# Performance work log

Hardware: AMD Instinct MI355X
Metric: run time of the kernel (lower is better)

The kernel has to match this reference:

```python
import jax, jax.numpy as jnp
import numpy as np

N = 50000
NUM_GRAPHS = 64
EPS = 1e-16  # PyG softmax denominator epsilon


def _gat_conv(x, src, dst, W, a_src, a_dst, b, heads, out_ch):
    n = x.shape[0]
    h = (x @ W).reshape(n, heads, out_ch)                    # [N,H,C]
    al_s = jnp.einsum('nhc,hc->nh', h, a_src)                # [N,H]
    al_d = jnp.einsum('nhc,hc->nh', h, a_dst)                # [N,H]
    e = jax.nn.leaky_relu(al_s[src] + al_d[dst], 0.2)        # [E,H]
    emax = jax.ops.segment_max(e, dst, num_segments=n)       # [N,H]
    ee = jnp.exp(e - emax[dst])
    den = jax.ops.segment_sum(ee, dst, num_segments=n)       # [N,H]
    alpha = ee / (den[dst] + EPS)                            # [E,H]
    msg = h[src] * alpha[:, :, None]                         # [E,H,C]
    out = jax.ops.segment_sum(msg, dst, num_segments=n)      # [N,H,C]
    return out.reshape(n, heads * out_ch) + b


def setup_inputs() -> dict:
    key = jax.random.key(0)
    ks = jax.random.split(key, 16)
    E = 250000
    x = jax.random.normal(ks[0], (N, 11), dtype=jnp.float32)
    edge_index = jax.random.randint(ks[1], (2, E), 0, N, dtype=jnp.int64)
    batch = jnp.sort(jax.random.randint(ks[2], (N,), 0, NUM_GRAPHS, dtype=jnp.int64))
    def glorot(k, shape):
        fan = shape[0] + shape[-1]
        return jax.random.uniform(k, shape, jnp.float32, -1.0, 1.0) * np.sqrt(6.0 / fan)
    return {
        'x': x, 'edge_index': edge_index, 'batch': batch,
        'W1': glorot(ks[3], (11, 8 * 128)),
        'a1s': glorot(ks[4], (8, 128)), 'a1d': glorot(ks[5], (8, 128)),
        'b1': jnp.zeros((8 * 128,), jnp.float32),
        'W2': glorot(ks[6], (1024, 8 * 64)),
        'a2s': glorot(ks[7], (8, 64)), 'a2d': glorot(ks[8], (8, 64)),
        'b2': jnp.zeros((8 * 64,), jnp.float32),
        'W3': glorot(ks[9], (512, 4 * 32)),
        'a3s': glorot(ks[10], (4, 32)), 'a3d': glorot(ks[11], (4, 32)),
        'b3': jnp.zeros((4 * 32,), jnp.float32),
        'Wout': glorot(ks[12], (128, 1)),
        'bout': jnp.zeros((1,), jnp.float32),
    }


def reference(x, edge_index, batch, W1, a1s, a1d, b1, W2, a2s, a2d, b2,
              W3, a3s, a3d, b3, Wout, bout):
    n = x.shape[0]
    # GATConv adds self-loops by default
    loop = jnp.arange(n, dtype=edge_index.dtype)
    src = jnp.concatenate([edge_index[0], loop])
    dst = jnp.concatenate([edge_index[1], loop])
    h = jax.nn.leaky_relu(_gat_conv(x, src, dst, W1, a1s, a1d, b1, 8, 128), 0.01)
    h = jax.nn.leaky_relu(_gat_conv(h, src, dst, W2, a2s, a2d, b2, 8, 64), 0.01)
    h = jax.nn.leaky_relu(_gat_conv(h, src, dst, W3, a3s, a3d, b3, 4, 32), 0.01)
    # global mean pool over graphs
    sums = jax.ops.segment_sum(h, batch, num_segments=NUM_GRAPHS)      # [G,128]
    cnt = jax.ops.segment_sum(jnp.ones((n,), h.dtype), batch, num_segments=NUM_GRAPHS)
    pooled = sums / jnp.maximum(cnt, 1.0)[:, None]
    return pooled @ Wout + bout                                        # [G,1]
```

## Files before the change

### kernel.cpp

```cpp
#include <hip/hip_runtime.h>

#define EPS 1e-16f

typedef __attribute__((ext_vector_type(8))) short short8;
typedef __attribute__((ext_vector_type(4))) float f32x4;

__device__ __forceinline__ float b2f(unsigned short u) {
    return __uint_as_float(((unsigned)u) << 16);
}
__device__ __forceinline__ unsigned short f2b(float f) {
    unsigned u = __float_as_uint(f);
    u += 0x7fffu + ((u >> 16) & 1u);
    return (unsigned short)(u >> 16);
}

typedef __attribute__((address_space(3))) void lds_vp;
typedef __attribute__((address_space(1))) const void glb_vp;
__device__ __forceinline__ void load_lds16(const unsigned short* g,
                                           unsigned short* l) {
    __builtin_amdgcn_global_load_lds((glb_vp*)g, (lds_vp*)l, 16, 0, 0);
}

__global__ void setup_kernel(const float* __restrict__ W1,
                             const float* __restrict__ W2,
                             const float* __restrict__ W3,
                             unsigned short* __restrict__ wt2,
                             unsigned short* __restrict__ wt3,
                             unsigned short* __restrict__ w1sk,
                             const float* __restrict__ a1s,
                             const float* __restrict__ a1d,
                             float* __restrict__ w_as,
                             float* __restrict__ w_ad, int* __restrict__ deg,
                             float* __restrict__ pool, int N, int GC, int WB,
                             int DB, int PB) {
    int b = blockIdx.x, t = threadIdx.x;
    if (b < WB) {
        int i = b * 256 + t;
        if (i < 1024 * 512) {
            int k = i / 512, n = i % 512;
            wt2[(size_t)n * 1024 + k] = f2b(W2[i]);
        } else if (i < 1024 * 512 + 512 * 128) {
            int j = i - 1024 * 512;
            int k = j / 128, n = j % 128;
            wt3[(size_t)n * 512 + k] = f2b(W3[j]);
        } else if (i < 1024 * 512 + 512 * 128 + 8 * 128 * 32) {
            int q = i - (1024 * 512 + 512 * 128);
            int h = q >> 12, rem = q & 4095;
            int c = rem >> 5, kk = rem & 31;
            int off = (h == 7) ? 16 : 0;
            float v = 0.f;
            int k = kk - off;
            if (k >= 0 && k < 11) v = W1[k * 1024 + h * 128 + c];
            w1sk[q] = f2b(v);
        }
    } else if (b < WB + DB) {
        int i = (b - WB) * 256 + t;
        if (i < N) deg[i] = 1;
    } else if (b < WB + DB + PB) {
        int i = (b - WB - DB) * 256 + t;
        if (i < GC) pool[i] = 0.f;
    } else {
        if (t < 88) {
            int h = t / 11, k = t % 11;
            float s = 0.f, d = 0.f;
            for (int c = 0; c < 128; c++) {
                float w = W1[k * 1024 + h * 128 + c];
                s += w * a1s[h * 128 + c];
                d += w * a1d[h * 128 + c];
            }
            w_as[h * 16 + k] = s;
            w_ad[h * 16 + k] = d;
        }
    }
}

__global__ void hist_al1_kernel(const int* __restrict__ ei, int E, int N,
                                int* __restrict__ deg,
                                const float* __restrict__ x,
                                const float* __restrict__ w_as,
                                const float* __restrict__ w_ad,
                                float* __restrict__ als,
                                float* __restrict__ ald, int EB) {
    int b = blockIdx.x, t = threadIdx.x;
    if (b < EB) {
        int e = b * 256 + t;
        if (e < E) {
            int d = ei[E + e];
            if ((unsigned)d < (unsigned)N) atomicAdd(&deg[d], 1);
        }
    } else {
        int i = (b - EB) * 256 + t;
        if (i < N * 8) {
            int n = i >> 3, h = i & 7;
            float s = 0.f, d = 0.f;
#pragma unroll
            for (int k = 0; k < 11; k++) {
                float xv = x[n * 11 + k];
                s += xv * w_as[h * 16 + k];
                d += xv * w_ad[h * 16 + k];
            }
            als[i] = s;
            ald[i] = d;
        }
    }
}

__global__ void scan_block_kernel(const int* __restrict__ deg,
                                  int* __restrict__ rowst,
                                  int* __restrict__ bsum, int N) {
    __shared__ int s[256];
    int t = threadIdx.x, b = blockIdx.x;
    int i = b * 256 + t;
    s[t] = (i < N) ? deg[i] : 0;
    __syncthreads();
    for (int o = 1; o < 256; o <<= 1) {
        int a = (t >= o) ? s[t - o] : 0;
        __syncthreads();
        s[t] += a;
        __syncthreads();
    }
    if (i < N) rowst[i + 1] = s[t];
    if (t == 255) bsum[b] = s[255];
}

__global__ void scan_top_kernel(const int* __restrict__ bsum,
                                int* __restrict__ boff, int NB) {
    __shared__ int psum[65];
    int t = threadIdx.x;
    int chunk = (NB + 63) / 64;
    int lo = t * chunk, hi = lo + chunk;
    if (lo > NB) lo = NB;
    if (hi > NB) hi = NB;
    int s = 0;
    for (int i = lo; i < hi; i++) s += bsum[i];
    psum[t + 1] = s;
    __syncthreads();
    if (t == 0) {
        psum[0] = 0;
        for (int i = 1; i <= 64; i++) psum[i] += psum[i - 1];
    }
    __syncthreads();
    int run = psum[t];
    for (int i = lo; i < hi; i++) {
        boff[i] = run;
        run += bsum[i];
    }
}

__global__ void scan_finish_kernel(int* __restrict__ rowst,
                                   const int* __restrict__ boff,
                                   const int* __restrict__ deg,
                                   int* __restrict__ srcs,
                                   int* __restrict__ cursor, int N) {
    int i = blockIdx.x * 256 + threadIdx.x;
    if (i == 0) rowst[0] = 0;
    if (i < N) {
        int incl = rowst[i + 1] + boff[blockIdx.x];
        rowst[i + 1] = incl;
        int st = incl - deg[i];
        srcs[st] = i;
        cursor[i] = st + 1;
    }
}

__global__ void scatter_kernel(const int* __restrict__ ei, int E, int N,
                               int* cursor, int* srcs) {
    int e = blockIdx.x * blockDim.x + threadIdx.x;
    if (e < E) {
        int d = ei[E + e];
        if ((unsigned)d < (unsigned)N) {
            int p = atomicAdd(&cursor[d], 1);
            int s = ei[e];
            if ((unsigned)s >= (unsigned)N) s = d;
            srcs[p] = s;
        }
    }
}

__global__ void agg1_fused(const float* __restrict__ x,
                           const float* __restrict__ als,
                           const float* __restrict__ ald,
                           const int* __restrict__ rowst,
                           const int* __restrict__ srcs,
                           unsigned short* __restrict__ A2, int N) {
    constexpr int MAXE = 64;
    __shared__ float sv[MAXE * 8];
    __shared__ float sx[MAXE * 12];
    int n = blockIdx.x;
    int t = threadIdx.x;
    int h = t >> 4, k = t & 15;
    int start = rowst[n], end = rowst[n + 1];
    int deg = end - start;
    float acc = 0.f;

    if (deg <= MAXE) {
        for (int p = t; p < deg * 8; p += 128) {
            int e = p >> 3, hh = p & 7;
            int s = srcs[start + e];
            float v = als[s * 8 + hh] + ald[n * 8 + hh];
            sv[e * 8 + hh] = v > 0.f ? v : 0.2f * v;
        }
        for (int p = t; p < deg * 16; p += 128) {
            int e = p >> 4, kx = p & 15;
            if (kx < 11)
                sx[e * 12 + kx] = x[(size_t)srcs[start + e] * 11 + kx];
        }
        __syncthreads();
        float m = -1e30f;
        for (int e = k; e < deg; e += 16) m = fmaxf(m, sv[e * 8 + h]);
#pragma unroll
        for (int o = 1; o < 16; o <<= 1) m = fmaxf(m, __shfl_xor(m, o));
        float ee[(MAXE + 15) / 16];
        float den = 0.f;
        {
            int kk = 0;
            for (int e = k; e < deg; e += 16, kk++) {
                float xv = expf(sv[e * 8 + h] - m);
                ee[kk] = xv;
                den += xv;
            }
        }
#pragma unroll
        for (int o = 1; o < 16; o <<= 1) den += __shfl_xor(den, o);
        float dinv = 1.0f / (den + EPS);
        {
            int kk = 0;
            for (int e = k; e < deg; e += 16, kk++)
                sv[e * 8 + h] = ee[kk] * dinv;
        }
        __syncthreads();
        const int CH = 4;
        for (int e = 0; e < deg; e += CH) {
            int mc = deg - e;
            if (mc > CH) mc = CH;
            float al[CH], xv[CH];
#pragma unroll
            for (int j = 0; j < CH; j++)
                if (j < mc) {
                    al[j] = sv[(e + j) * 8 + h];
                    xv[j] = (k < 11) ? sx[(e + j) * 12 + k] : 0.f;
                }
#pragma unroll
            for (int j = 0; j < CH; j++)
                if (j < mc) acc += al[j] * xv[j];
        }
    } else {
        float aldn = ald[n * 8 + h];
        float m = -1e30f;
        for (int idx = start + k; idx < end; idx += 16) {
            float v = als[srcs[idx] * 8 + h] + aldn;
            v = v > 0.f ? v : 0.2f * v;
            m = fmaxf(m, v);
        }
#pragma unroll
        for (int o = 1; o < 16; o <<= 1) m = fmaxf(m, __shfl_xor(m, o));
        float den = 0.f;
        for (int idx = start + k; idx < end; idx += 16) {
            float v = als[srcs[idx] * 8 + h] + aldn;
            v = v > 0.f ? v : 0.2f * v;
            den += expf(v - m);
        }
#pragma unroll
        for (int o = 1; o < 16; o <<= 1) den += __shfl_xor(den, o);
        float dinv = 1.0f / (den + EPS);
        for (int idx = start; idx < end; idx++) {
            int s = srcs[idx];
            float v = als[s * 8 + h] + aldn;
            v = v > 0.f ? v : 0.2f * v;
            float a = expf(v - m) * dinv;
            float xv = (k < 11) ? x[s * 11 + k] : 0.f;
            acc += a * xv;
        }
    }
    A2[(size_t)n * 128 + t] = f2b(acc);
}

template <bool EPI, int HB, int CC, bool SK>
__global__ __launch_bounds__(256) void gemm_mfma(
    const unsigned short* __restrict__ A, const unsigned short* __restrict__ Bt,
    unsigned short* __restrict__ C, const float* __restrict__ bias,
    const float* __restrict__ a_s, const float* __restrict__ a_d,
    float* __restrict__ als, float* __restrict__ ald, int H, int M, int N,
    int K, int lda) {
    int NX = gridDim.x;
    int bid = blockIdx.y * NX + blockIdx.x;
    int win = bid & (8 * NX - 1);
    int mg = bid / (8 * NX);
    int m_t = mg * 8 + (win & 7);
    int n_t = win >> 3;
    int bm = m_t * 128, bn = n_t * 128;
    if (bm >= M) return;

    union SMem {
        struct {
            unsigned short As[2][128 * 32];
            unsigned short Bs[2][128 * 32];
        } k;
        unsigned short Ct[128 * 132];
    };
    __shared__ __align__(16) SMem sm;
    auto& As = sm.k.As;
    auto& Bs = sm.k.Bs;
    auto& Ct = sm.Ct;

    int t = threadIdx.x;
    int w = t >> 6, lane = t & 63;
    int quad = lane >> 4, l16 = lane & 15;
    int wr = (w >> 1) * 64, wc = (w & 1) * 64;

    int kofs = 0;
    const unsigned short* Bb = Bt;
    if (SK) {
        kofs = n_t * 16;
        if (kofs > lda - 32) kofs = lda - 32;
        Bb = Bt + (size_t)n_t * 128 * 32;
    }

    int c0 = w * 128 + lane;
    int c1 = c0 + 64;
    int r0 = c0 >> 2, p0 = c0 & 3;
    int r1 = c1 >> 2, p1 = c1 & 3;
    int j0 = (p0 - (r0 >> 1)) & 3;
    int j1 = (p1 - (r1 >> 1)) & 3;
    int ga0 = bm + r0;
    if (ga0 >= M) ga0 = M - 1;
    int ga1 = bm + r1;
    if (ga1 >= M) ga1 = M - 1;
    const unsigned short* Ag0 = A + (size_t)ga0 * lda + kofs + j0 * 8;
    const unsigned short* Ag1 = A + (size_t)ga1 * lda + kofs + j1 * 8;
    size_t br0 = SK ? (size_t)r0 : (size_t)(bn + r0);
    size_t br1 = SK ? (size_t)r1 : (size_t)(bn + r1);
    const unsigned short* Bg0 = Bb + br0 * K + j0 * 8;
    const unsigned short* Bg1 = Bb + br1 * K + j1 * 8;

    auto stage = [&](int st, int k0) {
        load_lds16(Ag0 + k0, &As[st][(w * 128) * 8]);
        load_lds16(Ag1 + k0, &As[st][(w * 128 + 64) * 8]);
        load_lds16(Bg0 + k0, &Bs[st][(w * 128) * 8]);
        load_lds16(Bg1 + k0, &Bs[st][(w * 128 + 64) * 8]);
    };

    int aoff[4], boff4[4];
#pragma unroll
    for (int i = 0; i < 4; i++) {
        int ra = wr + i * 16 + l16;
        aoff[i] = ra * 32 + (((quad + (ra >> 1)) & 3) * 8);
        int rb = wc + i * 16 + l16;
        boff4[i] = rb * 32 + (((quad + (rb >> 1)) & 3) * 8);
    }

    f32x4 acc[4][4] = {};
    stage(0, 0);
    int st = 0;
    for (int k0 = 0; k0 < K; k0 += 32, st ^= 1) {
        __syncthreads();
        if (k0 + 32 < K) stage(st ^ 1, k0 + 32);
        short8 a[4], b[4];
#pragma unroll
        for (int mi = 0; mi < 4; mi++) a[mi] = *(const short8*)&As[st][aoff[mi]];
#pragma unroll
        for (int ni = 0; ni < 4; ni++) b[ni] = *(const short8*)&Bs[st][boff4[ni]];
#pragma unroll
        for (int mi = 0; mi < 4; mi++)
#pragma unroll
            for (int ni = 0; ni < 4; ni++)
                acc[mi][ni] = __builtin_amdgcn_mfma_f32_16x16x32_bf16(
                    a[mi], b[ni], acc[mi][ni], 0, 0, 0);
    }
    __syncthreads();

#pragma unroll
    for (int mi = 0; mi < 4; mi++) {
#pragma unroll
        for (int r = 0; r < 4; r++) {
            int rl = wr + mi * 16 + quad * 4 + r;
#pragma unroll
            for (int ni = 0; ni < 4; ni++) {
                int cl = wc + ni * 16 + l16;
                float v = acc[mi][ni][r];
                if (EPI) {
                    v += bias[bn + cl];
                    v = v > 0.f ? v : 0.01f * v;
                }
                Ct[rl * 132 + cl] = f2b(v);
            }
        }
    }
    __syncthreads();
#pragma unroll
    for (int p = 0; p < 16; p++) {
        int q = p * 256 + t;
        int row = q >> 5, c8 = q & 31;
        if (bm + row < M) {
            uint2 v = *(const uint2*)&Ct[row * 132 + c8 * 4];
            *(uint2*)&C[(size_t)(bm + row) * N + bn + c8 * 4] = v;
        }
    }
    if (HB > 0) {
        for (int pi = t; pi < 128 * HB; pi += 256) {
            int row = pi / HB, hl = pi % HB;
            if (bm + row >= M) continue;
            int hg = bn / CC + hl;
            const unsigned short* rp = &Ct[row * 132 + hl * CC];
            const float* asp = a_s + hg * CC;
            const float* adp = a_d + hg * CC;
            float s = 0.f, d = 0.f;
#pragma unroll
            for (int c = 0; c < CC; c++) {
                float v = b2f(rp[c]);
                s += v * asp[c];
                d += v * adp[c];
            }
            als[(size_t)(bm + row) * H + hg] = s;
            ald[(size_t)(bm + row) * H + hg] = d;
        }
    }
}

template <int HB, int CC>
__global__ __launch_bounds__(256, 2) void gemm_pipe(
    const unsigned short* __restrict__ A, const unsigned short* __restrict__ Bt,
    unsigned short* __restrict__ C, const float* __restrict__ a_s,
    const float* __restrict__ a_d, float* __restrict__ als,
    float* __restrict__ ald, int H, int M, int N, int K) {
    int NX = gridDim.x;
    int bid = blockIdx.y * NX + blockIdx.x;
    int win = bid & (8 * NX - 1);
    int mg = bid / (8 * NX);
    int m_t = mg * 8 + (win & 7);
    int n_t = win >> 3;
    int bm = m_t * 128, bn = n_t * 128;
    if (bm >= M) return;

    union SMem {
        struct {
            unsigned short As[2][128 * 64];
            unsigned short Bs[2][128 * 64];
        } k;
        unsigned short Ct[128 * 132];
    };
    __shared__ __align__(16) SMem sm;

    int t = threadIdx.x;
    int w = t >> 6, lane = t & 63;
    int quad = lane >> 4, l16 = lane & 15;
    int wr = (w >> 1) * 64, wc = (w & 1) * 64;

    int srow = lane >> 3;
    int gsl = (lane & 7) ^ srow;
    const unsigned short* Ag[4];
    const unsigned short* Bg[4];
#pragma unroll
    for (int j = 0; j < 4; j++) {
        int row = (j * 4 + w) * 8 + srow;
        int ga = bm + row;
        if (ga > M - 1) ga = M - 1;
        Ag[j] = A + (size_t)ga * K + gsl * 8;
        Bg[j] = Bt + (size_t)(bn + row) * K + gsl * 8;
    }
    auto stage = [&](int st, int kt) {
        int ko = kt * 64;
#pragma unroll
        for (int j = 0; j < 4; j++) {
            load_lds16(Ag[j] + ko, &sm.k.As[st][(j * 4 + w) * 512]);
            load_lds16(Bg[j] + ko, &sm.k.Bs[st][(j * 4 + w) * 512]);
        }
    };

    int arow[4], brow[4];
#pragma unroll
    for (int i = 0; i < 4; i++) {
        arow[i] = (wr + i * 16 + l16) * 64;
        brow[i] = (wc + i * 16 + l16) * 64;
    }
    int sw = l16 & 7;

    f32x4 acc[4][4] = {};
    int NT = K >> 6;
    stage(0, 0);
    if (NT > 1) stage(1, 1);
    for (int tt = 0; tt < NT; tt++) {
        int bb = tt & 1;
        if (tt + 1 < NT)
            asm volatile("s_waitcnt vmcnt(8)" ::: "memory");
        else
            asm volatile("s_waitcnt vmcnt(0)" ::: "memory");
        __builtin_amdgcn_s_barrier();
        __builtin_amdgcn_sched_barrier(0);
#pragma unroll
        for (int ks = 0; ks < 2; ks++) {
            short8 a[4], b[4];
            int so = ((ks * 4 + quad) ^ sw) * 8;
#pragma unroll
            for (int mi = 0; mi < 4; mi++)
                a[mi] = *(const short8*)&sm.k.As[bb][arow[mi] + so];
#pragma unroll
            for (int ni = 0; ni < 4; ni++)
                b[ni] = *(const short8*)&sm.k.Bs[bb][brow[ni] + so];
            __builtin_amdgcn_s_setprio(1);
#pragma unroll
            for (int mi = 0; mi < 4; mi++)
#pragma unroll
                for (int ni = 0; ni < 4; ni++)
                    acc[mi][ni] = __builtin_amdgcn_mfma_f32_16x16x32_bf16(
                        a[mi], b[ni], acc[mi][ni], 0, 0, 0);
            __builtin_amdgcn_s_setprio(0);
        }
        asm volatile("s_waitcnt lgkmcnt(0)" ::: "memory");
        __builtin_amdgcn_s_barrier();
        if (tt + 2 < NT) stage(bb, tt + 2);
    }
    __syncthreads();

#pragma unroll
    for (int mi = 0; mi < 4; mi++) {
#pragma unroll
        for (int r = 0; r < 4; r++) {
            int rl = wr + mi * 16 + quad * 4 + r;
#pragma unroll
            for (int ni = 0; ni < 4; ni++) {
                int cl = wc + ni * 16 + l16;
                sm.Ct[rl * 132 + cl] = f2b(acc[mi][ni][r]);
            }
        }
    }
    __syncthreads();
#pragma unroll
    for (int p = 0; p < 16; p++) {
        int q = p * 256 + t;
        int row = q >> 5, c8 = q & 31;
        if (bm + row < M) {
            uint2 v = *(const uint2*)&sm.Ct[row * 132 + c8 * 4];
            *(uint2*)&C[(size_t)(bm + row) * N + bn + c8 * 4] = v;
        }
    }
    if (HB > 0) {
        for (int pi = t; pi < 128 * HB; pi += 256) {
            int row = pi / HB, hl = pi % HB;
            if (bm + row >= M) continue;
            int hg = bn / CC + hl;
            const unsigned short* rp = &sm.Ct[row * 132 + hl * CC];
            const float* asp = a_s + hg * CC;
            const float* adp = a_d + hg * CC;
            float s = 0.f, d = 0.f;
#pragma unroll
            for (int c = 0; c < CC; c++) {
                float v = b2f(rp[c]);
                s += v * asp[c];
                d += v * adp[c];
            }
            als[(size_t)(bm + row) * H + hg] = s;
            ald[(size_t)(bm + row) * H + hg] = d;
        }
    }
}

template <int H, int C>
__global__ void agg_fused4(const unsigned short* __restrict__ hin,
                           const float* __restrict__ als,
                           const float* __restrict__ ald,
                           const int* __restrict__ rowst,
                           const int* __restrict__ srcs,
                           const float* __restrict__ bias,
                           unsigned short* __restrict__ out, int N) {
    constexpr int HC = H * C;
    constexpr int NT = HC / 8;
    constexpr int TPH = C / 8;
    constexpr int MAXE = 64;
    __shared__ float sv[MAXE * H];
    __shared__ int ssrc[MAXE];
    int n = blockIdx.x;
    int t = threadIdx.x;
    int c = t * 8;
    int hh = c / C;
    int li = (c % C) / 8;
    int start = rowst[n], end = rowst[n + 1];
    int deg = end - start;
    float acc[8] = {};

    if (deg <= MAXE) {
        for (int p = t; p < deg * H; p += NT) {
            int e = p / H, h = p % H;
            int s = srcs[start + e];
            if (h == 0) ssrc[e] = s;
            float v = als[s * H + h] + ald[n * H + h];
            sv[e * H + h] = v > 0.f ? v : 0.2f * v;
        }
        __syncthreads();
        float m = -1e30f;
        for (int e = li; e < deg; e += TPH) m = fmaxf(m, sv[e * H + hh]);
#pragma unroll
        for (int o = 1; o < TPH; o <<= 1) m = fmaxf(m, __shfl_xor(m, o));
        float ee[(MAXE + TPH - 1) / TPH];
        float den = 0.f;
        {
            int k = 0;
            for (int e = li; e < deg; e += TPH, k++) {
                float x = expf(sv[e * H + hh] - m);
                ee[k] = x;
                den += x;
            }
        }
#pragma unroll
        for (int o = 1; o < TPH; o <<= 1) den += __shfl_xor(den, o);
        float dinv = 1.0f / (den + EPS);
        {
            int k = 0;
            for (int e = li; e < deg; e += TPH, k++)
                sv[e * H + hh] = ee[k] * dinv;
        }
        __syncthreads();
        const int CH = 4;
        for (int e = 0; e < deg; e += CH) {
            int mc = deg - e;
            if (mc > CH) mc = CH;
            int ss[CH];
            float al[CH];
            short8 uv[CH];
#pragma unroll
            for (int j = 0; j < CH; j++)
                if (j < mc) {
                    ss[j] = ssrc[e + j];
                    al[j] = sv[(e + j) * H + hh];
                }
#pragma unroll
            for (int j = 0; j < CH; j++)
                if (j < mc)
                    uv[j] = *(const short8*)(hin + (size_t)ss[j] * HC + c);
#pragma unroll
            for (int j = 0; j < CH; j++)
                if (j < mc) {
                    float a = al[j];
#pragma unroll
                    for (int q = 0; q < 8; q++)
                        acc[q] += a * b2f((unsigned short)uv[j][q]);
                }
        }
    } else {
        float aldn = ald[n * H + hh];
        float m = -1e30f;
        for (int idx = start + li; idx < end; idx += TPH) {
            float v = als[srcs[idx] * H + hh] + aldn;
            v = v > 0.f ? v : 0.2f * v;
            m = fmaxf(m, v);
        }
#pragma unroll
        for (int o = 1; o < TPH; o <<= 1) m = fmaxf(m, __shfl_xor(m, o));
        float den = 0.f;
        for (int idx = start + li; idx < end; idx += TPH) {
            float v = als[srcs[idx] * H + hh] + aldn;
            v = v > 0.f ? v : 0.2f * v;
            den += expf(v - m);
        }
#pragma unroll
        for (int o = 1; o < TPH; o <<= 1) den += __shfl_xor(den, o);
        float dinv = 1.0f / (den + EPS);
        for (int idx = start; idx < end; idx++) {
            int s = srcs[idx];
            float v = als[s * H + hh] + aldn;
            v = v > 0.f ? v : 0.2f * v;
            float a = expf(v - m) * dinv;
            short8 uv = *(const short8*)(hin + (size_t)s * HC + c);
#pragma unroll
            for (int q = 0; q < 8; q++)
                acc[q] += a * b2f((unsigned short)uv[q]);
        }
    }
    short8 o8;
#pragma unroll
    for (int q = 0; q < 8; q++) {
        float v = acc[q] + bias[c + q];
        v = v > 0.f ? v : 0.01f * v;
        o8[q] = (short)f2b(v);
    }
    *(short8*)&out[(size_t)n * HC + c] = o8;
}

template <int H, int C>
__global__ void agg_fused2(const unsigned short* __restrict__ hin,
                           const float* __restrict__ als,
                           const float* __restrict__ ald,
                           const int* __restrict__ rowst,
                           const int* __restrict__ srcs,
                           const float* __restrict__ bias,
                           unsigned short* __restrict__ out, int N) {
    constexpr int HC = H * C;
    constexpr int NT = HC / 2;
    constexpr int TPH = C / 2;
    constexpr int MAXE = 64;
    __shared__ float sv[MAXE * H];
    __shared__ int ssrc[MAXE];
    int n = blockIdx.x;
    int t = threadIdx.x;
    int c = t * 2;
    int hh = c / C;
    int li = (c % C) / 2;
    int start = rowst[n], end = rowst[n + 1];
    int deg = end - start;
    float a0 = 0.f, a1 = 0.f;

    if (deg <= MAXE) {
        for (int p = t; p < deg * H; p += NT) {
            int e = p / H, h = p % H;
            int s = srcs[start + e];
            if (h == 0) ssrc[e] = s;
            float v = als[s * H + h] + ald[n * H + h];
            sv[e * H + h] = v > 0.f ? v : 0.2f * v;
        }
        __syncthreads();
        float m = -1e30f;
        for (int e = li; e < deg; e += TPH) m = fmaxf(m, sv[e * H + hh]);
#pragma unroll
        for (int o = 1; o < TPH; o <<= 1) m = fmaxf(m, __shfl_xor(m, o));
        float ee[(MAXE + TPH - 1) / TPH];
        float den = 0.f;
        {
            int k = 0;
            for (int e = li; e < deg; e += TPH, k++) {
                float x = expf(sv[e * H + hh] - m);
                ee[k] = x;
                den += x;
            }
        }
#pragma unroll
        for (int o = 1; o < TPH; o <<= 1) den += __shfl_xor(den, o);
        float dinv = 1.0f / (den + EPS);
        {
            int k = 0;
            for (int e = li; e < deg; e += TPH, k++)
                sv[e * H + hh] = ee[k] * dinv;
        }
        __syncthreads();
        const int CH = 4;
        for (int e = 0; e < deg; e += CH) {
            int mc = deg - e;
            if (mc > CH) mc = CH;
            int ss[CH];
            float al[CH];
            ushort2 uv[CH];
#pragma unroll
            for (int j = 0; j < CH; j++)
                if (j < mc) {
                    ss[j] = ssrc[e + j];
                    al[j] = sv[(e + j) * H + hh];
                }
#pragma unroll
            for (int j = 0; j < CH; j++)
                if (j < mc)
                    uv[j] = *(const ushort2*)(hin + (size_t)ss[j] * HC + c);
#pragma unroll
            for (int j = 0; j < CH; j++)
                if (j < mc) {
                    a0 += al[j] * b2f(uv[j].x);
                    a1 += al[j] * b2f(uv[j].y);
                }
        }
    } else {
        float aldn = ald[n * H + hh];
        float m = -1e30f;
        for (int idx = start + li; idx < end; idx += TPH) {
            float v = als[srcs[idx] * H + hh] + aldn;
            v = v > 0.f ? v : 0.2f * v;
            m = fmaxf(m, v);
        }
#pragma unroll
        for (int o = 1; o < TPH; o <<= 1) m = fmaxf(m, __shfl_xor(m, o));
        float den = 0.f;
        for (int idx = start + li; idx < end; idx += TPH) {
            float v = als[srcs[idx] * H + hh] + aldn;
            v = v > 0.f ? v : 0.2f * v;
            den += expf(v - m);
        }
#pragma unroll
        for (int o = 1; o < TPH; o <<= 1) den += __shfl_xor(den, o);
        float dinv = 1.0f / (den + EPS);
        const int CH = 4;
        for (int idx = start; idx < end; idx += CH) {
            int mc = end - idx;
            if (mc > CH) mc = CH;
            int ss[CH];
            float lv[CH];
            ushort2 uv[CH];
#pragma unroll
            for (int j = 0; j < CH; j++)
                if (j < mc) ss[j] = srcs[idx + j];
#pragma unroll
            for (int j = 0; j < CH; j++)
                if (j < mc) lv[j] = als[ss[j] * H + hh];
#pragma unroll
            for (int j = 0; j < CH; j++)
                if (j < mc)
                    uv[j] = *(const ushort2*)(hin + (size_t)ss[j] * HC + c);
#pragma unroll
            for (int j = 0; j < CH; j++)
                if (j < mc) {
                    float v = lv[j] + aldn;
                    v = v > 0.f ? v : 0.2f * v;
                    float a = expf(v - m) * dinv;
                    a0 += a * b2f(uv[j].x);
                    a1 += a * b2f(uv[j].y);
                }
        }
    }
    float v0 = a0 + bias[c], v1 = a1 + bias[c + 1];
    ushort2 o;
    o.x = f2b(v0 > 0.f ? v0 : 0.01f * v0);
    o.y = f2b(v1 > 0.f ? v1 : 0.01f * v1);
    *(ushort2*)&out[(size_t)n * HC + c] = o;
}

__global__ void pool_partial_kernel(const unsigned short* __restrict__ h3,
                                    const int* __restrict__ batch,
                                    float* __restrict__ pool, int N, int G) {
    int lo = blockIdx.x * 128;
    int hi = lo + 128;
    if (hi > N) hi = N;
    if (lo >= N) return;
    int t = threadIdx.x;
    int cur = batch[lo];
    float acc = 0.f;
    for (int n = lo; n < hi; n++) {
        int g = batch[n];
        if (g != cur) {
            if ((unsigned)cur < (unsigned)G) atomicAdd(&pool[cur * 128 + t], acc);
            acc = 0.f;
            cur = g;
        }
        acc += b2f(h3[(size_t)n * 128 + t]);
    }
    if ((unsigned)cur < (unsigned)G) atomicAdd(&pool[cur * 128 + t], acc);
}

__global__ void head_kernel(const float* __restrict__ pool,
                            const int* __restrict__ batch,
                            const float* __restrict__ Wout,
                            const float* __restrict__ bout,
                            float* __restrict__ out, int N) {
    int g = blockIdx.x;
    int t = threadIdx.x;
    int lo, hi;
    {
        int a = 0, b = N;
        while (a < b) { int mid = (a + b) >> 1; if (batch[mid] < g) a = mid + 1; else b = mid; }
        lo = a;
        a = lo; b = N;
        while (a < b) { int mid = (a + b) >> 1; if (batch[mid] < g + 1) a = mid + 1; else b = mid; }
        hi = a;
    }
    float c = (float)(hi - lo);
    c = c > 1.f ? c : 1.f;
    float v = (pool[g * 128 + t] / c) * Wout[t];
    for (int o = 32; o; o >>= 1) v += __shfl_xor(v, o);
    __shared__ float partial[2];
    if ((t & 63) == 0) partial[t >> 6] = v;
    __syncthreads();
    if (t == 0) out[g] = partial[0] + partial[1] + bout[0];
}

extern "C" void kernel_launch(void* const* d_in, const int* in_sizes, int n_in,
                              void* d_out, int out_size, void* d_ws,
                              size_t ws_size, hipStream_t stream) {
    const float* x = (const float*)d_in[0];
    const int* ei = (const int*)d_in[1];
    const int* batch = (const int*)d_in[2];
    const float* W1 = (const float*)d_in[3];
    const float* a1s = (const float*)d_in[4];
    const float* a1d = (const float*)d_in[5];
    const float* b1 = (const float*)d_in[6];
    const float* W2 = (const float*)d_in[7];
    const float* a2s = (const float*)d_in[8];
    const float* a2d = (const float*)d_in[9];
    const float* b2 = (const float*)d_in[10];
    const float* W3 = (const float*)d_in[11];
    const float* a3s = (const float*)d_in[12];
    const float* a3d = (const float*)d_in[13];
    const float* b3 = (const float*)d_in[14];
    const float* Wout = (const float*)d_in[15];
    const float* bout = (const float*)d_in[16];
    float* out = (float*)d_out;

    const int N = in_sizes[0] / 11;
    const int E = in_sizes[1] / 2;
    const int Etot = E + N;
    const int G = out_size;
    const int NB = (N + 255) / 256;
    const int MT = ((N + 127) / 128 + 7) / 8 * 8;

    char* ws = (char*)d_ws;
    size_t off = 0;
    auto alloc = [&](size_t bytes) -> void* {
        void* p = ws + off;
        off += (bytes + 255) & ~(size_t)255;
        return p;
    };
    unsigned short* buf1 = (unsigned short*)alloc((size_t)N * 1024 * 2);
    unsigned short* buf2 = (unsigned short*)alloc((size_t)N * 1024 * 2);
    float* als = (float*)alloc((size_t)N * 8 * 4);
    float* ald = (float*)alloc((size_t)N * 8 * 4);
    int* rowst = (int*)alloc((size_t)(N + 1) * 4);
    int* cursor = (int*)alloc((size_t)N * 4);
    int* srcs = (int*)alloc((size_t)Etot * 4);
    int* deg = (int*)alloc((size_t)N * 4);
    int* bsum = (int*)alloc((size_t)NB * 4);
    int* boff = (int*)alloc((size_t)NB * 4);
    float* pool = (float*)alloc((size_t)G * 128 * 4);
    unsigned short* aggx = (unsigned short*)alloc((size_t)N * 128 * 2);
    unsigned short* w1sk = (unsigned short*)alloc((size_t)8 * 128 * 32 * 2);
    unsigned short* wt2 = (unsigned short*)alloc((size_t)1024 * 512 * 2);
    unsigned short* wt3 = (unsigned short*)alloc((size_t)512 * 128 * 2);
    float* w_as = (float*)alloc(8 * 16 * 4);
    float* w_ad = (float*)alloc(8 * 16 * 4);

    int nb = (N + 255) / 256;
    int eb = (E + 255) / 256;

    const int WTOT = 1024 * 512 + 512 * 128 + 8 * 128 * 32;
    const int WB = (WTOT + 255) / 256;
    const int PB = (G * 128 + 255) / 256;
    setup_kernel<<<WB + nb + PB + 1, 256, 0, stream>>>(
        W1, W2, W3, wt2, wt3, w1sk, a1s, a1d, w_as, w_ad, deg, pool, N,
        G * 128, WB, nb, PB);

    const int AB = (N * 8 + 255) / 256;
    hist_al1_kernel<<<eb + AB, 256, 0, stream>>>(ei, E, N, deg, x, w_as, w_ad,
                                                 als, ald, eb);

    scan_block_kernel<<<NB, 256, 0, stream>>>(deg, rowst, bsum, N);
    scan_top_kernel<<<1, 64, 0, stream>>>(bsum, boff, NB);
    scan_finish_kernel<<<NB, 256, 0, stream>>>(rowst, boff, deg, srcs, cursor,
                                               N);
    scatter_kernel<<<eb, 256, 0, stream>>>(ei, E, N, cursor, srcs);

    agg1_fused<<<N, 128, 0, stream>>>(x, als, ald, rowst, srcs, aggx, N);
    gemm_mfma<true, 0, 1, true><<<dim3(8, MT), 256, 0, stream>>>(
        aggx, w1sk, buf2, b1, nullptr, nullptr, nullptr, nullptr, 0, N, 1024,
        32, 128);

    gemm_pipe<2, 64><<<dim3(4, MT), 256, 0, stream>>>(
        buf2, wt2, buf1, a2s, a2d, als, ald, 8, N, 512, 1024);
    agg_fused4<8, 64><<<N, 64, 0, stream>>>(buf1, als, ald, rowst, srcs, b2,
                                            buf2, N);

    gemm_pipe<4, 32><<<dim3(1, MT), 256, 0, stream>>>(
        buf2, wt3, buf1, a3s, a3d, als, ald, 4, N, 128, 512);
    agg_fused2<4, 32><<<N, 64, 0, stream>>>(buf1, als, ald, rowst, srcs, b3,
                                            buf2, N);

    pool_partial_kernel<<<(N + 127) / 128, 128, 0, stream>>>(buf2, batch, pool,
                                                             N, G);
    head_kernel<<<G, 128, 0, stream>>>(pool, batch, Wout, bout, out, N);
}
```

Before: 416.9 us.

## Fuse global mean pooling into final GAT aggregation via replicated atomic pools

Removes the separate pooling kernel and the bf16 write of the last layer's activations. The last aggregation kernel now applies bias and leaky-ReLU, then atomically adds each node's features into one of 8 replicated per-graph pool buffers chosen by node index. The head kernel sums the 8 replicas before computing the mean and output. This trades a kernel launch and a memory round trip for many fine-grained float atomics with possible contention, and it changes the summation order.

```diff
diff --git a/kernel.cpp b/kernel.cpp
--- a/kernel.cpp
+++ b/kernel.cpp
@@ -683,7 +683,8 @@
                            const int* __restrict__ rowst,
                            const int* __restrict__ srcs,
                            const float* __restrict__ bias,
-                           unsigned short* __restrict__ out, int N) {
+                           const int* __restrict__ batch,
+                           float* __restrict__ pool, int GC, int N) {
     constexpr int HC = H * C;
     constexpr int NT = HC / 2;
     constexpr int TPH = C / 2;
@@ -803,39 +804,19 @@
         }
     }
     float v0 = a0 + bias[c], v1 = a1 + bias[c + 1];
-    ushort2 o;
-    o.x = f2b(v0 > 0.f ? v0 : 0.01f * v0);
-    o.y = f2b(v1 > 0.f ? v1 : 0.01f * v1);
-    *(ushort2*)&out[(size_t)n * HC + c] = o;
-}
-
-__global__ void pool_partial_kernel(const unsigned short* __restrict__ h3,
-                                    const int* __restrict__ batch,
-                                    float* __restrict__ pool, int N, int G) {
-    int lo = blockIdx.x * 128;
-    int hi = lo + 128;
-    if (hi > N) hi = N;
-    if (lo >= N) return;
-    int t = threadIdx.x;
-    int cur = batch[lo];
-    float acc = 0.f;
-    for (int n = lo; n < hi; n++) {
-        int g = batch[n];
-        if (g != cur) {
-            if ((unsigned)cur < (unsigned)G) atomicAdd(&pool[cur * 128 + t], acc);
-            acc = 0.f;
-            cur = g;
-        }
-        acc += b2f(h3[(size_t)n * 128 + t]);
-    }
-    if ((unsigned)cur < (unsigned)G) atomicAdd(&pool[cur * 128 + t], acc);
+    v0 = v0 > 0.f ? v0 : 0.01f * v0;
+    v1 = v1 > 0.f ? v1 : 0.01f * v1;
+    int g = batch[n];
+    float* pp = pool + (size_t)(n & 7) * GC + g * 128;
+    atomicAdd(&pp[c], v0);
+    atomicAdd(&pp[c + 1], v1);
 }
 
 __global__ void head_kernel(const float* __restrict__ pool,
                             const int* __restrict__ batch,
                             const float* __restrict__ Wout,
                             const float* __restrict__ bout,
-                            float* __restrict__ out, int N) {
+                            float* __restrict__ out, int GC, int N) {
     int g = blockIdx.x;
     int t = threadIdx.x;
     int lo, hi;
@@ -849,7 +830,10 @@
     }
     float c = (float)(hi - lo);
     c = c > 1.f ? c : 1.f;
-    float v = (pool[g * 128 + t] / c) * Wout[t];
+    float s = 0.f;
+#pragma unroll
+    for (int p = 0; p < 8; p++) s += pool[(size_t)p * GC + g * 128 + t];
+    float v = (s / c) * Wout[t];
     for (int o = 32; o; o >>= 1) v += __shfl_xor(v, o);
     __shared__ float partial[2];
     if ((t & 63) == 0) partial[t >> 6] = v;
@@ -883,6 +867,7 @@
     const int E = in_sizes[1] / 2;
     const int Etot = E + N;
     const int G = out_size;
+    const int GC = G * 128;
     const int NB = (N + 255) / 256;
     const int MT = ((N + 127) / 128 + 7) / 8 * 8;
 
@@ -903,7 +888,7 @@
     int* deg = (int*)alloc((size_t)N * 4);
     int* bsum = (int*)alloc((size_t)NB * 4);
     int* boff = (int*)alloc((size_t)NB * 4);
-    float* pool = (float*)alloc((size_t)G * 128 * 4);
+    float* pool = (float*)alloc((size_t)GC * 8 * 4);
     unsigned short* aggx = (unsigned short*)alloc((size_t)N * 128 * 2);
     unsigned short* w1sk = (unsigned short*)alloc((size_t)8 * 128 * 32 * 2);
     unsigned short* wt2 = (unsigned short*)alloc((size_t)1024 * 512 * 2);
@@ -916,10 +901,10 @@
 
     const int WTOT = 1024 * 512 + 512 * 128 + 8 * 128 * 32;
     const int WB = (WTOT + 255) / 256;
-    const int PB = (G * 128 + 255) / 256;
+    const int PB = (GC * 8 + 255) / 256;
     setup_kernel<<<WB + nb + PB + 1, 256, 0, stream>>>(
         W1, W2, W3, wt2, wt3, w1sk, a1s, a1d, w_as, w_ad, deg, pool, N,
-        G * 128, WB, nb, PB);
+        GC * 8, WB, nb, PB);
 
     const int AB = (N * 8 + 255) / 256;
     hist_al1_kernel<<<eb + AB, 256, 0, stream>>>(ei, E, N, deg, x, w_as, w_ad,
@@ -944,9 +929,7 @@
     gemm_pipe<4, 32><<<dim3(1, MT), 256, 0, stream>>>(
         buf2, wt3, buf1, a3s, a3d, als, ald, 4, N, 128, 512);
     agg_fused2<4, 32><<<N, 64, 0, stream>>>(buf1, als, ald, rowst, srcs, b3,
-                                            buf2, N);
-
-    pool_partial_kernel<<<(N + 127) / 128, 128, 0, stream>>>(buf2, batch, pool,
-                                                             N, G);
-    head_kernel<<<G, 128, 0, stream>>>(pool, batch, Wout, bout, out, N);
-}
+                                            batch, pool, GC, N);
+
+    head_kernel<<<G, 128, 0, stream>>>(pool, batch, Wout, bout, out, GC, N);
+}
```

New measurement: 502.5 us. 1.21x slower.
